# Kernel tuning notes

Hardware: AMD Instinct MI355X
Metric: run time of the kernel (lower is better)

Reference implementation:

```python
import jax, jax.numpy as jnp
import numpy as np

QK_DIM = 64
ATTN_BETA = 1.0 / QK_DIM ** 0.5  # default beta = 1/sqrt(qk_dim)


def setup_inputs() -> dict:
    key = jax.random.key(0)
    k1, k2, k3, k4 = jax.random.split(key, 4)
    B, K, D = 8, 1024, 768
    H, Z = 12, 64
    M = int(D * 4.0)
    g = jax.random.normal(k1, (B, K, D), dtype=jnp.float32)
    wq = jax.random.normal(k2, (H, Z, D), dtype=jnp.float32) * 0.02
    wk = jax.random.normal(k3, (H, Z, D), dtype=jnp.float32) * 0.02
    w_hn = jax.random.normal(k4, (M, D), dtype=jnp.float32) * (1.0 / np.sqrt(D))
    beta_hn = jnp.ones((1,), dtype=jnp.float32) * 0.01
    return {"g": g, "wq": wq, "wk": wk, "w_hn": w_hn, "beta_hn": beta_hn}


def reference(g, wq, wk, w_hn, beta_hn):
    # Attention energy: q,k = per-head projections; E = -1/beta * sum logsumexp(beta * QK^T)
    q = jnp.einsum('bkd,hzd->bkhz', g, wq)  # [B,K,H,Z]
    k = jnp.einsum('bkd,hzd->bkhz', g, wk)  # [B,K,H,Z]
    A = jnp.einsum('bqhz,bkhz->bhqk', q, k)  # [B,H,Q,K]
    attn_e = -1.0 / ATTN_BETA * jnp.sum(jax.nn.logsumexp(ATTN_BETA * A, axis=-1))
    # Hopfield energy: E = -1/beta_hn * sum logsumexp(beta_hn * g W^T)
    h = beta_hn * jnp.einsum('bkd,md->bkm', g, w_hn)  # [B,K,M]
    hn_e = -1.0 / beta_hn * jnp.sum(jax.nn.logsumexp(h, axis=-1))  # shape (1,)
    return attn_e + hn_e  # shape (1,) matching torch broadcast
```

## Files before the change

### kernel.cpp

```cpp
#include <hip/hip_runtime.h>
#include <hip/hip_bf16.h>
#include <stdint.h>
#include <stddef.h>

typedef float  f32x4  __attribute__((ext_vector_type(4)));
typedef float  f32x16 __attribute__((ext_vector_type(16)));
typedef int    i32x8  __attribute__((ext_vector_type(8)));
typedef unsigned char u8;

#define LOG2E  1.44269504f
#define QSCALE 0.18033688f
#define WSC    16.0f
#define IWSC   0.0625f
#define QSTORE 0.36067376f
#define KSTORE 0.5f
#define SCALE_A_M8 0x77777777
#define SCALE_ONE  0x7F7F7F7F

__device__ __forceinline__ void gld_lds16(const void* gptr, void* lptr) {
    __builtin_amdgcn_global_load_lds(
        (const __attribute__((address_space(1))) unsigned int*)gptr,
        (__attribute__((address_space(3))) unsigned int*)lptr,
        16, 0, 0);
}

__global__ void cast_all(const float* __restrict__ g, const float* __restrict__ wq,
                         const float* __restrict__ wk, const float* __restrict__ whn,
                         u8* __restrict__ g_f8, u8* __restrict__ Wcat,
                         float* __restrict__ sums, float* __restrict__ out) {
    int b = blockIdx.x, t = threadIdx.x;
    if (b < 104) {
        float4 z = {0.f, 0.f, 0.f, 0.f};
        *(float4*)(sums + (b * 256 + t) * 4) = z;
        if (b == 0 && t == 0) out[0] = 0.f;
    }
    const float* src; u8* dst; int off; float sc;
    if (b < 6144)      { src = g;   dst = g_f8;           off = 0;    sc = 1.0f; }
    else if (b < 6720) { src = wq;  dst = Wcat;           off = 6144; sc = WSC;  }
    else if (b < 7296) { src = wk;  dst = Wcat + 589824;  off = 6720; sc = WSC;  }
    else               { src = whn; dst = Wcat + 1179648; off = 7296; sc = WSC;  }
    int i = ((b - off) * 256 + t) * 4;
    float4 v = *(const float4*)(src + i);
    int p = __builtin_amdgcn_cvt_pk_fp8_f32(sc * v.x, sc * v.y, 0, false);
    p     = __builtin_amdgcn_cvt_pk_fp8_f32(sc * v.z, sc * v.w, p, true);
    *(int*)(dst + i) = p;
}

__global__ void gemm_fused(const u8* __restrict__ A, const u8* __restrict__ Bm,
                           u8* __restrict__ qkh, float* __restrict__ rowsum,
                           const float* __restrict__ beta_p) {
    __shared__ __align__(16) u8 As[128 * 128];
    __shared__ __align__(16) u8 Bs[128 * 128];
    const int t = threadIdx.x;
    const int w = t >> 6, l = t & 63;
    const int wm = (w >> 1) * 64, wn = (w & 1) * 64;
    const int tile_m = blockIdx.x * 128;
    const int tile_n = blockIdx.y * 128;

    f32x4 acc[4][4];
#pragma unroll
    for (int i = 0; i < 4; i++)
#pragma unroll
        for (int j = 0; j < 4; j++)
#pragma unroll
            for (int q = 0; q < 4; q++) acc[i][j][q] = 0.f;

    const int srow = t >> 3;
    const int sswz = (t & 7) ^ (srow & 7);
    const u8* gA = A  + (size_t)(tile_m + srow) * 768 + sswz * 16;
    const u8* gB = Bm + (size_t)(tile_n + srow) * 768 + sswz * 16;

    const int fr = l & 15, fg = l >> 4;
    const int s0 = ((2 * fg)     ^ (fr & 7)) * 16;
    const int s1 = ((2 * fg + 1) ^ (fr & 7)) * 16;

    for (int k0 = 0; k0 < 768; k0 += 128) {
#pragma unroll
        for (int i = 0; i < 4; i++) {
            gld_lds16(gA + (size_t)i * 32 * 768 + k0, As + (i * 256 + t) * 16);
            gld_lds16(gB + (size_t)i * 32 * 768 + k0, Bs + (i * 256 + t) * 16);
        }
        __builtin_amdgcn_s_waitcnt(0);
        __syncthreads();

        union F8 { uint4 q[2]; i32x8 v; };
        i32x8 af[4], bfr[4];
#pragma unroll
        for (int i = 0; i < 4; i++) {
            const u8* ra = As + (wm + i * 16 + fr) * 128;
            const u8* rb = Bs + (wn + i * 16 + fr) * 128;
            F8 ua, ub;
            ua.q[0] = *(const uint4*)(ra + s0);
            ua.q[1] = *(const uint4*)(ra + s1);
            ub.q[0] = *(const uint4*)(rb + s0);
            ub.q[1] = *(const uint4*)(rb + s1);
            af[i] = ua.v; bfr[i] = ub.v;
        }
#pragma unroll
        for (int i = 0; i < 4; i++)
#pragma unroll
            for (int j = 0; j < 4; j++)
                acc[i][j] = __builtin_amdgcn_mfma_scale_f32_16x16x128_f8f6f4(
                    af[i], bfr[j], acc[i][j], 0, 0, 0, SCALE_ONE, 0, SCALE_ONE);
        __syncthreads();
    }

    const int cr = fg * 4, cc = fr;

    if (tile_n < 1536) {
        const int tt = (tile_n >= 768);
        const int hh = (tile_n - tt * 768 + wn) >> 6;
        const int bb = tile_m >> 10;
        const int m7 = tile_m & 1023;
        const float sc = tt ? KSTORE : QSTORE;
        u8* base = qkh + ((size_t)((bb * 12 + hh) * 2 + tt) << 16);
#pragma unroll
        for (int i = 0; i < 4; i++)
#pragma unroll
            for (int r = 0; r < 4; r++) {
                int kr = m7 + wm + i * 16 + cr + r;
                int u = kr >> 1, p4 = (kr & 1) * 4, u7 = u & 7;
                u8* rowp = base + (size_t)u * 128;
#pragma unroll
                for (int j = 0; j < 4; j++) {
                    int pv = __builtin_amdgcn_cvt_pk_fp8_f32(sc * acc[i][j][r], 0.f, 0, false);
                    rowp[((p4 + j) ^ u7) * 16 + cc] = (u8)(pv & 0xFF);
                }
            }
    } else {
        const float sc2 = beta_p[0] * LOG2E * IWSC;
#pragma unroll
        for (int i = 0; i < 4; i++)
#pragma unroll
            for (int r = 0; r < 4; r++) {
                float s = 0.f;
#pragma unroll
                for (int j = 0; j < 4; j++) s += __builtin_amdgcn_exp2f(sc2 * acc[i][j][r]);
                s += __shfl_xor(s, 1, 16);
                s += __shfl_xor(s, 2, 16);
                s += __shfl_xor(s, 4, 16);
                s += __shfl_xor(s, 8, 16);
                if ((l & 15) == 0)
                    atomicAdd(&rowsum[tile_m + wm + i * 16 + cr + r], s);
            }
    }
}

__global__ void __launch_bounds__(256, 4)
attn_energy(const u8* __restrict__ qkh, float* __restrict__ arow) {
    __shared__ __align__(16) u8 Sk[32768];
    const int t = threadIdx.x, w = t >> 6, l = t & 63;
    const int qt = blockIdx.x >> 1, kh = blockIdx.x & 1;
    const int h = blockIdx.y, b = blockIdx.z;
    const u8* qp = qkh + ((size_t)((b * 12 + h) * 2 + 0) << 16) + qt * 8192;
    const u8* kp = qkh + ((size_t)((b * 12 + h) * 2 + 1) << 16) + kh * 32768;

#pragma unroll
    for (int i = 0; i < 8; i++)
        gld_lds16(kp + (i * 256 + t) * 16, Sk + (i * 256 + t) * 16);

    const int ln = l & 31, lh = l >> 5;
    union F8x32 { uint4 q[2]; i32x8 v; };

    const int rA = w * 32 + ln, uA = rA >> 1, u7A = uA & 7;
    const int sA = (rA & 1) * 4 + lh * 2;
    F8x32 ua;
    ua.q[0] = *(const uint4*)(qp + uA * 128 + ((sA)     ^ u7A) * 16);
    ua.q[1] = *(const uint4*)(qp + uA * 128 + ((sA + 1) ^ u7A) * 16);

    float rs[16];
#pragma unroll
    for (int r = 0; r < 16; r++) rs[r] = 0.f;

    __builtin_amdgcn_s_waitcnt(0);
    __syncthreads();

#pragma unroll 2
    for (int nt = 0; nt < 16; nt++) {
        const int rB = nt * 32 + ln, uB = rB >> 1, u7B = uB & 7;
        const int sB = (rB & 1) * 4 + lh * 2;
        F8x32 ub;
        ub.q[0] = *(const uint4*)(Sk + uB * 128 + ((sB)     ^ u7B) * 16);
        ub.q[1] = *(const uint4*)(Sk + uB * 128 + ((sB + 1) ^ u7B) * 16);
        f32x16 acc;
#pragma unroll
        for (int q = 0; q < 16; q++) acc[q] = 0.f;
        acc = __builtin_amdgcn_mfma_scale_f32_32x32x64_f8f6f4(
            ua.v, ub.v, acc, 0, 0, 0, SCALE_A_M8, 0, SCALE_ONE);
#pragma unroll
        for (int r = 0; r < 16; r++) rs[r] += __builtin_amdgcn_exp2f(acc[r]);
    }

    const int rowbase = (b * 12 + h) * 1024 + qt * 128 + w * 32 + lh * 4;
#pragma unroll
    for (int r = 0; r < 16; r++) {
        float v = rs[r];
        v += __shfl_xor(v, 1, 32);
        v += __shfl_xor(v, 2, 32);
        v += __shfl_xor(v, 4, 32);
        v += __shfl_xor(v, 8, 32);
        v += __shfl_xor(v, 16, 32);
        if (ln == 0)
            atomicAdd(&arow[rowbase + (r & 3) + 8 * (r >> 2)], v);
    }
}

__global__ void finalize(const float* __restrict__ sums, const float* __restrict__ beta_p,
                         float* __restrict__ out) {
    __shared__ float wpart[4];
    const int t = threadIdx.x, w = t >> 6, l = t & 63;
    const int i = blockIdx.x * 256 + t;
    float v;
    if (i < 8192) v = (-1.f / beta_p[0]) * __logf(sums[i]);
    else          v = -8.f * __logf(sums[i]);
    for (int o = 32; o > 0; o >>= 1) v += __shfl_down(v, o, 64);
    if (l == 0) wpart[w] = v;
    __syncthreads();
    if (t == 0) atomicAdd(out, wpart[0] + wpart[1] + wpart[2] + wpart[3]);
}

extern "C" void kernel_launch(void* const* d_in, const int* in_sizes, int n_in,
                              void* d_out, int out_size, void* d_ws, size_t ws_size,
                              hipStream_t stream) {
    const float* g    = (const float*)d_in[0];
    const float* wq   = (const float*)d_in[1];
    const float* wk   = (const float*)d_in[2];
    const float* w_hn = (const float*)d_in[3];
    const float* beta = (const float*)d_in[4];
    float* out = (float*)d_out;

    char* ws = (char*)d_ws;
    u8*    g_f8   = (u8*)(ws);
    u8*    Wcat   = (u8*)(ws + 6291456);
    u8*    qkh    = (u8*)(ws + 9830400);
    float* sums   = (float*)(ws + 22413312);
    float* rowsum = sums;
    float* arow   = sums + 8192;

    cast_all<<<9600, 256, 0, stream>>>(g, wq, wk, w_hn, g_f8, Wcat, sums, out);

    dim3 gg(64, 36);
    gemm_fused<<<gg, 256, 0, stream>>>(g_f8, Wcat, qkh, rowsum, beta);

    dim3 ga(16, 12, 8);
    attn_energy<<<ga, 256, 0, stream>>>(qkh, arow);

    finalize<<<416, 256, 0, stream>>>(sums, beta, out);
}
```

Baseline: 148.1 us.

## Double-buffer GEMM K-loop with 64-wide stages and switch to 32x32x64 MFMA

```diff
diff --git a/kernel.cpp b/kernel.cpp
--- a/kernel.cpp
+++ b/kernel.cpp
@@ -49,99 +49,113 @@
 __global__ void gemm_fused(const u8* __restrict__ A, const u8* __restrict__ Bm,
                            u8* __restrict__ qkh, float* __restrict__ rowsum,
                            const float* __restrict__ beta_p) {
-    __shared__ __align__(16) u8 As[128 * 128];
-    __shared__ __align__(16) u8 Bs[128 * 128];
+    __shared__ __align__(16) u8 As[2][8192];
+    __shared__ __align__(16) u8 Bs[2][8192];
     const int t = threadIdx.x;
     const int w = t >> 6, l = t & 63;
     const int wm = (w >> 1) * 64, wn = (w & 1) * 64;
     const int tile_m = blockIdx.x * 128;
     const int tile_n = blockIdx.y * 128;
 
-    f32x4 acc[4][4];
-#pragma unroll
-    for (int i = 0; i < 4; i++)
-#pragma unroll
-        for (int j = 0; j < 4; j++)
-#pragma unroll
-            for (int q = 0; q < 4; q++) acc[i][j][q] = 0.f;
-
-    const int srow = t >> 3;
-    const int sswz = (t & 7) ^ (srow & 7);
-    const u8* gA = A  + (size_t)(tile_m + srow) * 768 + sswz * 16;
-    const u8* gB = Bm + (size_t)(tile_n + srow) * 768 + sswz * 16;
-
-    const int fr = l & 15, fg = l >> 4;
-    const int s0 = ((2 * fg)     ^ (fr & 7)) * 16;
-    const int s1 = ((2 * fg + 1) ^ (fr & 7)) * 16;
-
-    for (int k0 = 0; k0 < 768; k0 += 128) {
-#pragma unroll
-        for (int i = 0; i < 4; i++) {
-            gld_lds16(gA + (size_t)i * 32 * 768 + k0, As + (i * 256 + t) * 16);
-            gld_lds16(gB + (size_t)i * 32 * 768 + k0, Bs + (i * 256 + t) * 16);
-        }
+    f32x16 acc[2][2];
+#pragma unroll
+    for (int i = 0; i < 2; i++)
+#pragma unroll
+        for (int j = 0; j < 2; j++)
+#pragma unroll
+            for (int q = 0; q < 16; q++) acc[i][j][q] = 0.f;
+
+    const u8* gA[2]; const u8* gB[2];
+#pragma unroll
+    for (int i = 0; i < 2; i++) {
+        int sl = i * 256 + t, u = sl >> 3;
+        int su = (t & 7) ^ (u & 7);
+        int row = 2 * u + (su >> 2), ks = su & 3;
+        gA[i] = A  + (size_t)(tile_m + row) * 768 + ks * 16;
+        gB[i] = Bm + (size_t)(tile_n + row) * 768 + ks * 16;
+    }
+
+    const int ln = l & 31, lh = l >> 5;
+    const int sb = (ln & 1) * 4 + lh * 2;
+    union F8x32 { uint4 q[2]; i32x8 v; };
+
+#pragma unroll
+    for (int i = 0; i < 2; i++) {
+        gld_lds16(gA[i], As[0] + (i * 256 + t) * 16);
+        gld_lds16(gB[i], Bs[0] + (i * 256 + t) * 16);
+    }
+
+#pragma unroll
+    for (int kk = 0; kk < 12; kk++) {
+        const int p = kk & 1;
         __builtin_amdgcn_s_waitcnt(0);
         __syncthreads();
-
-        union F8 { uint4 q[2]; i32x8 v; };
-        i32x8 af[4], bfr[4];
-#pragma unroll
-        for (int i = 0; i < 4; i++) {
-            const u8* ra = As + (wm + i * 16 + fr) * 128;
-            const u8* rb = Bs + (wn + i * 16 + fr) * 128;
-            F8 ua, ub;
-            ua.q[0] = *(const uint4*)(ra + s0);
-            ua.q[1] = *(const uint4*)(ra + s1);
-            ub.q[0] = *(const uint4*)(rb + s0);
-            ub.q[1] = *(const uint4*)(rb + s1);
-            af[i] = ua.v; bfr[i] = ub.v;
+        if (kk < 11) {
+#pragma unroll
+            for (int i = 0; i < 2; i++) {
+                gld_lds16(gA[i] + (kk + 1) * 64, As[p ^ 1] + (i * 256 + t) * 16);
+                gld_lds16(gB[i] + (kk + 1) * 64, Bs[p ^ 1] + (i * 256 + t) * 16);
+            }
         }
-#pragma unroll
-        for (int i = 0; i < 4; i++)
-#pragma unroll
-            for (int j = 0; j < 4; j++)
-                acc[i][j] = __builtin_amdgcn_mfma_scale_f32_16x16x128_f8f6f4(
-                    af[i], bfr[j], acc[i][j], 0, 0, 0, SCALE_ONE, 0, SCALE_ONE);
-        __syncthreads();
-    }
-
-    const int cr = fg * 4, cc = fr;
+        i32x8 af[2], bf[2];
+#pragma unroll
+        for (int mi = 0; mi < 2; mi++) {
+            int rA = wm + mi * 32 + ln, uA = rA >> 1, u7 = uA & 7;
+            F8x32 x;
+            x.q[0] = *(const uint4*)(As[p] + uA * 128 + ((sb)     ^ u7) * 16);
+            x.q[1] = *(const uint4*)(As[p] + uA * 128 + ((sb + 1) ^ u7) * 16);
+            af[mi] = x.v;
+            int rB = wn + mi * 32 + ln, uB = rB >> 1, v7 = uB & 7;
+            F8x32 y;
+            y.q[0] = *(const uint4*)(Bs[p] + uB * 128 + ((sb)     ^ v7) * 16);
+            y.q[1] = *(const uint4*)(Bs[p] + uB * 128 + ((sb + 1) ^ v7) * 16);
+            bf[mi] = y.v;
+        }
+#pragma unroll
+        for (int mi = 0; mi < 2; mi++)
+#pragma unroll
+            for (int nj = 0; nj < 2; nj++)
+                acc[mi][nj] = __builtin_amdgcn_mfma_scale_f32_32x32x64_f8f6f4(
+                    af[mi], bf[nj], acc[mi][nj], 0, 0, 0, SCALE_ONE, 0, SCALE_ONE);
+    }
 
     if (tile_n < 1536) {
         const int tt = (tile_n >= 768);
-        const int hh = (tile_n - tt * 768 + wn) >> 6;
         const int bb = tile_m >> 10;
         const int m7 = tile_m & 1023;
         const float sc = tt ? KSTORE : QSTORE;
-        u8* base = qkh + ((size_t)((bb * 12 + hh) * 2 + tt) << 16);
-#pragma unroll
-        for (int i = 0; i < 4; i++)
-#pragma unroll
-            for (int r = 0; r < 4; r++) {
-                int kr = m7 + wm + i * 16 + cr + r;
-                int u = kr >> 1, p4 = (kr & 1) * 4, u7 = u & 7;
-                u8* rowp = base + (size_t)u * 128;
-#pragma unroll
-                for (int j = 0; j < 4; j++) {
-                    int pv = __builtin_amdgcn_cvt_pk_fp8_f32(sc * acc[i][j][r], 0.f, 0, false);
-                    rowp[((p4 + j) ^ u7) * 16 + cc] = (u8)(pv & 0xFF);
+#pragma unroll
+        for (int mi = 0; mi < 2; mi++)
+#pragma unroll
+            for (int nj = 0; nj < 2; nj++) {
+                const int colbase = tile_n - tt * 768 + wn + nj * 32;
+                const int hh = colbase >> 6;
+                const int z  = (colbase & 63) + ln;
+                u8* base = qkh + ((size_t)((bb * 12 + hh) * 2 + tt) << 16);
+#pragma unroll
+                for (int r = 0; r < 16; r++) {
+                    int kr = m7 + wm + mi * 32 + (r & 3) + 8 * (r >> 2) + 4 * lh;
+                    int u = kr >> 1, u7 = u & 7;
+                    int slot = ((kr & 1) * 4 + (z >> 4)) ^ u7;
+                    int pv = __builtin_amdgcn_cvt_pk_fp8_f32(sc * acc[mi][nj][r], 0.f, 0, false);
+                    base[(size_t)u * 128 + slot * 16 + (z & 15)] = (u8)(pv & 0xFF);
                 }
             }
     } else {
         const float sc2 = beta_p[0] * LOG2E * IWSC;
 #pragma unroll
-        for (int i = 0; i < 4; i++)
-#pragma unroll
-            for (int r = 0; r < 4; r++) {
-                float s = 0.f;
-#pragma unroll
-                for (int j = 0; j < 4; j++) s += __builtin_amdgcn_exp2f(sc2 * acc[i][j][r]);
-                s += __shfl_xor(s, 1, 16);
-                s += __shfl_xor(s, 2, 16);
-                s += __shfl_xor(s, 4, 16);
-                s += __shfl_xor(s, 8, 16);
-                if ((l & 15) == 0)
-                    atomicAdd(&rowsum[tile_m + wm + i * 16 + cr + r], s);
+        for (int mi = 0; mi < 2; mi++)
+#pragma unroll
+            for (int r = 0; r < 16; r++) {
+                float s = __builtin_amdgcn_exp2f(sc2 * acc[mi][0][r])
+                        + __builtin_amdgcn_exp2f(sc2 * acc[mi][1][r]);
+                s += __shfl_xor(s, 1, 32);
+                s += __shfl_xor(s, 2, 32);
+                s += __shfl_xor(s, 4, 32);
+                s += __shfl_xor(s, 8, 32);
+                s += __shfl_xor(s, 16, 32);
+                if (ln == 0)
+                    atomicAdd(&rowsum[tile_m + wm + mi * 32 + (r & 3) + 8 * (r >> 2) + 4 * lh], s);
             }
     }
 }
```

Result: slower. 161.1 us (+8.7%).
